# Kernel tuning notes

Hardware: AMD Instinct MI355X
Metric: run time of the kernel (lower is better)

## Reference

```python
import jax, jax.numpy as jnp
import numpy as np

HEADS = 16
IN_FEATURE = 1024
D_HEAD = IN_FEATURE // HEADS
N = 32768


def setup_inputs() -> dict:
    key = jax.random.key(0)
    ks = jax.random.split(key, 16)
    s_in = 1.0 / np.sqrt(IN_FEATURE)
    inp = {
        "Q": jax.random.normal(ks[0], (N, IN_FEATURE), jnp.float32),
        "K": jax.random.normal(ks[1], (N, IN_FEATURE), jnp.float32),
        "V": jax.random.normal(ks[2], (N, IN_FEATURE), jnp.float32),
        "lq_w": jax.random.uniform(ks[3], (D_HEAD, IN_FEATURE), jnp.float32, -s_in, s_in),
        "lq_b": jax.random.uniform(ks[4], (D_HEAD,), jnp.float32, -s_in, s_in),
        "lk1_w": jax.random.uniform(ks[5], (D_HEAD, IN_FEATURE), jnp.float32, -s_in, s_in),
        "lk1_b": jax.random.uniform(ks[6], (D_HEAD,), jnp.float32, -s_in, s_in),
        "lk2_w": jax.random.uniform(ks[7], (D_HEAD, IN_FEATURE), jnp.float32, -s_in, s_in),
        "lk2_b": jax.random.uniform(ks[8], (D_HEAD,), jnp.float32, -s_in, s_in),
        "lv1_w": jax.random.uniform(ks[9], (D_HEAD, IN_FEATURE), jnp.float32, -s_in, s_in),
        "lv1_b": jax.random.uniform(ks[10], (D_HEAD,), jnp.float32, -s_in, s_in),
        "lv2_w": jax.random.uniform(ks[11], (D_HEAD, IN_FEATURE), jnp.float32, -s_in, s_in),
        "lv2_b": jax.random.uniform(ks[12], (D_HEAD,), jnp.float32, -s_in, s_in),
        "lh_w": jax.random.uniform(ks[13], (IN_FEATURE, IN_FEATURE), jnp.float32, -s_in, s_in),
        "lh_b": jax.random.uniform(ks[14], (IN_FEATURE,), jnp.float32, -s_in, s_in),
    }
    return inp


def _linear(x, w, b):
    # torch nn.Linear: x @ w.T + b
    return x @ w.T + b


def reference(Q, K, V, lq_w, lq_b, lk1_w, lk1_b, lk2_w, lk2_b,
              lv1_w, lv1_b, lv2_w, lv2_b, lh_w, lh_b):
    # The original loops over heads but the body is loop-invariant:
    # every iteration produces the identical [N, D_HEAD] tensor.
    # Compute once and tile HEADS times (same math as the torch code).
    q = _linear(Q, lq_w, lq_b)     # [N, Dh]
    k1 = _linear(K, lk1_w, lk1_b)  # [N, Dh]
    k2 = _linear(V, lk2_w, lk2_b)
    v1 = _linear(K, lv1_w, lv1_b)
    v2 = _linear(V, lv2_w, lv2_b)

    kv1 = jnp.sum(q * k1, axis=1, keepdims=True)  # [N, 1]
    kv2 = jnp.sum(q * k2, axis=1, keepdims=True)  # [N, 1]
    m = jnp.maximum(kv1, kv2)
    e1 = jnp.exp(kv1 - m)
    e2 = jnp.exp(kv2 - m)
    denom = e1 + e2
    head = (e1 / denom) * v1 + (e2 / denom) * v2   # [N, Dh]

    concat_head = jnp.tile(head, (1, HEADS))       # [N, IN_FEATURE]
    return _linear(concat_head, lh_w, lh_b)
```

## Files before the change

kernel.cpp:

```cpp
#include <hip/hip_runtime.h>
#include <hip/hip_bf16.h>

typedef __attribute__((ext_vector_type(4))) float f32x4;
typedef __attribute__((ext_vector_type(8))) short bf16x8;

#define MFMA(a, b, c) __builtin_amdgcn_mfma_f32_16x16x32_bf16(a, b, c, 0, 0, 0)

__device__ __forceinline__ short f2bf(float f) {
    union { float f; unsigned u; } v; v.f = f;
    unsigned r = v.u + 0x7fffu + ((v.u >> 16) & 1u);
    return (short)(r >> 16);
}

__device__ __forceinline__ short f2bf_h(float f) {
    __hip_bfloat16 h = __float2bfloat16(f);
    return *reinterpret_cast<const short*>(&h);
}

__device__ __forceinline__ bf16x8 cvt8h(f32x4 a, f32x4 b) {
    bf16x8 r;
    #pragma unroll
    for (int i = 0; i < 4; ++i) {
        r[i]     = f2bf_h(a[i]);
        r[4 + i] = f2bf_h(b[i]);
    }
    return r;
}

__device__ __forceinline__ void gll16(const void* g, const void* l) {
    __builtin_amdgcn_global_load_lds(
        (const __attribute__((address_space(1))) void*)g,
        (__attribute__((address_space(3))) void*)l, 16, 0, 0);
}

#define WS_WEFF   327680
#define WS_BALL_B 786432

__global__ __launch_bounds__(256) void prep_kernel(
        const float* __restrict__ lq_w, const float* __restrict__ lk1_w,
        const float* __restrict__ lk2_w, const float* __restrict__ lv1_w,
        const float* __restrict__ lv2_w, const float* __restrict__ lh_w,
        const float* __restrict__ lq_b, const float* __restrict__ lk1_b,
        const float* __restrict__ lk2_b, const float* __restrict__ lv1_b,
        const float* __restrict__ lv2_b,
        short* __restrict__ W_all, short* __restrict__ weff,
        float* __restrict__ b_all) {
    int t = blockIdx.x * 256 + threadIdx.x;
    if (t < 327680) {
        int row = t >> 10, col = t & 1023;
        int seg = row >> 6, sr = row & 63;
        const float* src = (seg == 0) ? lq_w : (seg == 1) ? lk1_w
                         : (seg == 2) ? lv1_w : (seg == 3) ? lk2_w : lv2_w;
        W_all[t] = f2bf(src[sr * 1024 + col]);
    } else if (t < 393216) {
        int i = t - 327680;
        int j = i >> 6, d = i & 63;
        float s = 0.f;
        #pragma unroll
        for (int h = 0; h < 16; ++h) s += lh_w[j * 1024 + h * 64 + d];
        weff[i] = f2bf(s);
    } else if (t < 393536) {
        int i = t - 393216;
        int seg = i >> 6, si = i & 63;
        const float* src = (seg == 0) ? lq_b : (seg == 1) ? lk1_b
                         : (seg == 2) ? lv1_b : (seg == 3) ? lk2_b : lv2_b;
        b_all[i] = src[si];
    }
}

__global__ __launch_bounds__(256, 3) void fused_kernel(
        const float* __restrict__ Q, const float* __restrict__ K,
        const float* __restrict__ V, const short* __restrict__ W_all,
        const float* __restrict__ b_all, const short* __restrict__ weff,
        const float* __restrict__ lh_b, float* __restrict__ out) {
    __shared__ __align__(16) char lds[49152];
    const int tid  = threadIdx.x;
    const int wid  = tid >> 6;
    const int lane = tid & 63;
    const int lrow = lane & 15;
    const int lkg  = lane >> 4;
    const int RB   = blockIdx.x * 32;

    const float* asrc[3];
    int adst[3];
    #pragma unroll
    for (int u = 0; u < 3; ++u) {
        const int idx  = wid * 3 + u;
        const int inp  = idx >> 2;
        const int rg   = idx & 3;
        const int row  = rg * 8 + (lane >> 3);
        const int cell = lane & 7;
        const float* base = (inp == 0) ? Q : (inp == 1) ? K : V;
        asrc[u] = base + (size_t)(RB + row) * 1024 + ((cell ^ (row & 7)) << 2);
        adst[u] = inp * 4096 + rg * 1024;
    }

    const short* wsrc[5];
    #pragma unroll
    for (int j = 0; j < 5; ++j)
        wsrc[j] = W_all + (size_t)(j * 64 + wid * 16 + lrow) * 1024 + lkg * 8;

    f32x4 acc[2][5];
    #pragma unroll
    for (int rt = 0; rt < 2; ++rt)
        #pragma unroll
        for (int j = 0; j < 5; ++j) acc[rt][j] = (f32x4){0.f, 0.f, 0.f, 0.f};

    bf16x8 wE[5], wO[5];
    const int r7 = lrow & 7;
    const int c0 = ((lkg * 2)     ^ r7) << 4;
    const int c1 = ((lkg * 2 + 1) ^ r7) << 4;

    #pragma unroll
    for (int u = 0; u < 3; ++u) gll16(asrc[u], lds + adst[u]);
    #pragma unroll
    for (int j = 0; j < 5; ++j)
        asm volatile("global_load_dwordx4 %0, %1, off"
                     : "=&v"(wE[j]) : "v"(wsrc[j]) : "memory");
    #pragma unroll
    for (int j = 0; j < 5; ++j)
        asm volatile("global_load_dwordx4 %0, %1, off"
                     : "=&v"(wO[j]) : "v"(wsrc[j] + 32) : "memory");
    #pragma unroll
    for (int u = 0; u < 3; ++u) gll16(asrc[u] + 32, lds + 12288 + adst[u]);
    #pragma unroll
    for (int u = 0; u < 3; ++u) gll16(asrc[u] + 64, lds + 24576 + adst[u]);
    asm volatile("s_waitcnt vmcnt(11)" ::: "memory");
    __builtin_amdgcn_sched_barrier(0);
    __builtin_amdgcn_s_barrier();
    __builtin_amdgcn_sched_barrier(0);

#define BODY(c, wb)                                                            \
    {                                                                          \
        const char* Ab = lds + ((c) & 3) * 12288;                              \
        bf16x8 fq[2], fk[2], fv[2];                                            \
        _Pragma("unroll")                                                      \
        for (int rt = 0; rt < 2; ++rt) {                                       \
            const int ro = (rt * 16 + lrow) * 128;                             \
            f32x4 q0 = *(const f32x4*)(Ab + ro + c0);                          \
            f32x4 q1 = *(const f32x4*)(Ab + ro + c1);                          \
            f32x4 k0 = *(const f32x4*)(Ab + 4096 + ro + c0);                   \
            f32x4 k1 = *(const f32x4*)(Ab + 4096 + ro + c1);                   \
            f32x4 v0 = *(const f32x4*)(Ab + 8192 + ro + c0);                   \
            f32x4 v1 = *(const f32x4*)(Ab + 8192 + ro + c1);                   \
            fq[rt] = cvt8h(q0, q1);                                            \
            fk[rt] = cvt8h(k0, k1);                                            \
            fv[rt] = cvt8h(v0, v1);                                            \
        }                                                                      \
        _Pragma("unroll")                                                      \
        for (int rt = 0; rt < 2; ++rt) {                                       \
            acc[rt][0] = MFMA(fq[rt], wb[0], acc[rt][0]);                      \
            acc[rt][1] = MFMA(fk[rt], wb[1], acc[rt][1]);                      \
            acc[rt][2] = MFMA(fk[rt], wb[2], acc[rt][2]);                      \
            acc[rt][3] = MFMA(fv[rt], wb[3], acc[rt][3]);                      \
            acc[rt][4] = MFMA(fv[rt], wb[4], acc[rt][4]);                      \
        }                                                                      \
        const int kcW = ((c) + 2 < 32) ? ((c) + 2) : 31;                       \
        _Pragma("unroll")                                                      \
        for (int j = 0; j < 5; ++j)                                            \
            asm volatile("global_load_dwordx4 %0, %1, off"                     \
                         : "=&v"(wb[j]) : "v"(wsrc[j] + kcW * 32) : "memory"); \
        const int kcA = ((c) + 3 < 32) ? ((c) + 3) : 31;                       \
        char* Db = lds + (((c) + 3) & 3) * 12288;                              \
        _Pragma("unroll")                                                      \
        for (int u = 0; u < 3; ++u)                                            \
            gll16(asrc[u] + kcA * 32, Db + adst[u]);                           \
        __builtin_amdgcn_sched_barrier(0);                                     \
        asm volatile("s_waitcnt vmcnt(11)" ::: "memory");                      \
        __builtin_amdgcn_sched_barrier(0);                                     \
        __builtin_amdgcn_s_barrier();                                          \
        __builtin_amdgcn_sched_barrier(0);                                     \
    }

    #pragma unroll 1
    for (int cc = 0; cc < 32; cc += 2) {
        BODY(cc, wE);
        BODY(cc + 1, wO);
    }
#undef BODY

    asm volatile("s_waitcnt vmcnt(0)" ::: "memory");
    __builtin_amdgcn_sched_barrier(0);
    __syncthreads();

    float* epi = (float*)lds;
    #pragma unroll
    for (int rt = 0; rt < 2; ++rt)
        #pragma unroll
        for (int j = 0; j < 5; ++j) {
            const int col = j * 64 + wid * 16 + lrow;
            const float bb = b_all[col];
            #pragma unroll
            for (int i = 0; i < 4; ++i)
                epi[(rt * 16 + lkg * 4 + i) * 324 + col] = acc[rt][j][i] + bb;
        }
    __syncthreads();

    const int r = tid >> 3;
    const int p = tid & 7;
    const float* er = epi + r * 324;
    float p1 = 0.f, p2 = 0.f;
    #pragma unroll
    for (int jj = 0; jj < 8; ++jj) {
        const float qv = er[p * 8 + jj];
        p1 += qv * er[64  + p * 8 + jj];
        p2 += qv * er[192 + p * 8 + jj];
    }
    p1 += __shfl_xor(p1, 1, 64); p1 += __shfl_xor(p1, 2, 64); p1 += __shfl_xor(p1, 4, 64);
    p2 += __shfl_xor(p2, 1, 64); p2 += __shfl_xor(p2, 2, 64); p2 += __shfl_xor(p2, 4, 64);
    const float mx = fmaxf(p1, p2);
    const float e1 = __expf(p1 - mx);
    const float e2 = __expf(p2 - mx);
    const float inv = 1.f / (e1 + e2);
    const float g1 = e1 * inv, g2 = e2 * inv;

    short* head_s = (short*)(lds + 41472);
    #pragma unroll
    for (int d = 0; d < 8; ++d) {
        const float h = g1 * er[128 + p * 8 + d] + g2 * er[256 + p * 8 + d];
        head_s[r * 72 + p * 8 + d] = f2bf_h(h);
    }
    __syncthreads();

    bf16x8 ha[2][2];
    #pragma unroll
    for (int rt = 0; rt < 2; ++rt) {
        ha[rt][0] = *(const bf16x8*)(head_s + (rt * 16 + lrow) * 72 + lkg * 8);
        ha[rt][1] = *(const bf16x8*)(head_s + (rt * 16 + lrow) * 72 + 32 + lkg * 8);
    }
    const int cgbase = wid * 256;
    #pragma unroll 4
    for (int jt = 0; jt < 16; ++jt) {
        const int col = cgbase + jt * 16 + lrow;
        const float bb = lh_b[col];
        const short* wp = weff + col * 64 + lkg * 8;
        const bf16x8 w0 = *(const bf16x8*)(wp);
        const bf16x8 w1 = *(const bf16x8*)(wp + 32);
        #pragma unroll
        for (int rt = 0; rt < 2; ++rt) {
            f32x4 a = {bb, bb, bb, bb};
            a = MFMA(ha[rt][0], w0, a);
            a = MFMA(ha[rt][1], w1, a);
            #pragma unroll
            for (int i = 0; i < 4; ++i)
                out[(size_t)(RB + rt * 16 + lkg * 4 + i) * 1024 + col] = a[i];
        }
    }
}

extern "C" void kernel_launch(void* const* d_in, const int* in_sizes, int n_in,
                              void* d_out, int out_size, void* d_ws, size_t ws_size,
                              hipStream_t stream) {
    const float* Q     = (const float*)d_in[0];
    const float* K     = (const float*)d_in[1];
    const float* V     = (const float*)d_in[2];
    const float* lq_w  = (const float*)d_in[3];
    const float* lq_b  = (const float*)d_in[4];
    const float* lk1_w = (const float*)d_in[5];
    const float* lk1_b = (const float*)d_in[6];
    const float* lk2_w = (const float*)d_in[7];
    const float* lk2_b = (const float*)d_in[8];
    const float* lv1_w = (const float*)d_in[9];
    const float* lv1_b = (const float*)d_in[10];
    const float* lv2_w = (const float*)d_in[11];
    const float* lv2_b = (const float*)d_in[12];
    const float* lh_w  = (const float*)d_in[13];
    const float* lh_b  = (const float*)d_in[14];
    float* out = (float*)d_out;

    short* W_all = (short*)d_ws;
    short* weff  = W_all + WS_WEFF;
    float* b_all = (float*)((char*)d_ws + WS_BALL_B);

    prep_kernel<<<1538, 256, 0, stream>>>(lq_w, lk1_w, lk2_w, lv1_w, lv2_w, lh_w,
                                          lq_b, lk1_b, lk2_b, lv1_b, lv2_b,
                                          W_all, weff, b_all);
    fused_kernel<<<1024, 256, 0, stream>>>(Q, K, V, W_all, b_all, weff, lh_b, out);
}
```

Before: 163.7 us.

## Pre-swizzle projection weights into MFMA fragment order and reorder prefetch issue

The prep kernel now writes the five projection weight matrices in bf16 MFMA fragment order, so each lane's 16-byte weight fragment for a k-chunk sits contiguously and a wave reads one coalesced block per chunk instead of strided rows. The main loop now issues the activation LDS prefetch at the top of each step, before the LDS reads and MFMAs, with the weight register prefetch issued after. The vmcnt wait thresholds are changed to match the new issue order. This aims to cut weight-load transaction overhead and overlap activation loads better, at the risk of getting the counter bookkeeping wrong.

After: 140.0 us. -14.5%, faster.

```diff
diff --git a/kernel.cpp b/kernel.cpp
--- a/kernel.cpp
+++ b/kernel.cpp
@@ -43,21 +43,29 @@
         const float* __restrict__ lq_b, const float* __restrict__ lk1_b,
         const float* __restrict__ lk2_b, const float* __restrict__ lv1_b,
         const float* __restrict__ lv2_b,
-        short* __restrict__ W_all, short* __restrict__ weff,
+        short* __restrict__ W_frag, short* __restrict__ weff,
         float* __restrict__ b_all) {
     int t = blockIdx.x * 256 + threadIdx.x;
     if (t < 327680) {
-        int row = t >> 10, col = t & 1023;
-        int seg = row >> 6, sr = row & 63;
-        const float* src = (seg == 0) ? lq_w : (seg == 1) ? lk1_w
-                         : (seg == 2) ? lv1_w : (seg == 3) ? lk2_w : lv2_w;
-        W_all[t] = f2bf(src[sr * 1024 + col]);
+        const int e    = t & 7;
+        const int u16  = t >> 3;
+        const int lane = u16 & 63;
+        const int tl   = u16 >> 6;
+        const int c    = tl / 20;
+        const int tt   = tl - c * 20;
+        const int j    = tt >> 2;
+        const int wd   = tt & 3;
+        const int lrow = lane & 15;
+        const int lkg  = lane >> 4;
+        const float* src = (j == 0) ? lq_w : (j == 1) ? lk1_w
+                         : (j == 2) ? lv1_w : (j == 3) ? lk2_w : lv2_w;
+        W_frag[t] = f2bf(src[(wd * 16 + lrow) * 1024 + c * 32 + lkg * 8 + e]);
     } else if (t < 393216) {
         int i = t - 327680;
-        int j = i >> 6, d = i & 63;
+        int jj = i >> 6, d = i & 63;
         float s = 0.f;
         #pragma unroll
-        for (int h = 0; h < 16; ++h) s += lh_w[j * 1024 + h * 64 + d];
+        for (int h = 0; h < 16; ++h) s += lh_w[jj * 1024 + h * 64 + d];
         weff[i] = f2bf(s);
     } else if (t < 393536) {
         int i = t - 393216;
@@ -70,7 +78,7 @@
 
 __global__ __launch_bounds__(256, 3) void fused_kernel(
         const float* __restrict__ Q, const float* __restrict__ K,
-        const float* __restrict__ V, const short* __restrict__ W_all,
+        const float* __restrict__ V, const short* __restrict__ W_frag,
         const float* __restrict__ b_all, const short* __restrict__ weff,
         const float* __restrict__ lh_b, float* __restrict__ out) {
     __shared__ __align__(16) char lds[49152];
@@ -85,20 +93,20 @@
     int adst[3];
     #pragma unroll
     for (int u = 0; u < 3; ++u) {
-        const int idx  = wid * 3 + u;
-        const int inp  = idx >> 2;
-        const int rg   = idx & 3;
-        const int row  = rg * 8 + (lane >> 3);
-        const int cell = lane & 7;
+        const int i   = wid * 3 + u;
+        const int inp = i >> 2;
+        const int rg  = i & 3;
+        const int row = rg * 8 + (lane >> 3);
+        const int gc  = (lane & 7) ^ (row & 7);
         const float* base = (inp == 0) ? Q : (inp == 1) ? K : V;
-        asrc[u] = base + (size_t)(RB + row) * 1024 + ((cell ^ (row & 7)) << 2);
+        asrc[u] = base + (size_t)(RB + row) * 1024 + gc * 4;
         adst[u] = inp * 4096 + rg * 1024;
     }
 
     const short* wsrc[5];
     #pragma unroll
     for (int j = 0; j < 5; ++j)
-        wsrc[j] = W_all + (size_t)(j * 64 + wid * 16 + lrow) * 1024 + lkg * 8;
+        wsrc[j] = W_frag + (size_t)((j * 4 + wid) * 64 + lane) * 8;
 
     f32x4 acc[2][5];
     #pragma unroll
@@ -106,33 +114,41 @@
         #pragma unroll
         for (int j = 0; j < 5; ++j) acc[rt][j] = (f32x4){0.f, 0.f, 0.f, 0.f};
 
-    bf16x8 wE[5], wO[5];
+    bf16x8 wA[5], wB[5];
     const int r7 = lrow & 7;
     const int c0 = ((lkg * 2)     ^ r7) << 4;
     const int c1 = ((lkg * 2 + 1) ^ r7) << 4;
 
+#define GLD4(dst, p) \
+    asm volatile("global_load_dwordx4 %0, %1, off" : "=&v"(dst) : "v"(p) : "memory")
+
     #pragma unroll
     for (int u = 0; u < 3; ++u) gll16(asrc[u], lds + adst[u]);
     #pragma unroll
-    for (int j = 0; j < 5; ++j)
-        asm volatile("global_load_dwordx4 %0, %1, off"
-                     : "=&v"(wE[j]) : "v"(wsrc[j]) : "memory");
-    #pragma unroll
-    for (int j = 0; j < 5; ++j)
-        asm volatile("global_load_dwordx4 %0, %1, off"
-                     : "=&v"(wO[j]) : "v"(wsrc[j] + 32) : "memory");
-    #pragma unroll
     for (int u = 0; u < 3; ++u) gll16(asrc[u] + 32, lds + 12288 + adst[u]);
     #pragma unroll
+    for (int j = 0; j < 5; ++j) GLD4(wA[j], wsrc[j]);
+    #pragma unroll
     for (int u = 0; u < 3; ++u) gll16(asrc[u] + 64, lds + 24576 + adst[u]);
-    asm volatile("s_waitcnt vmcnt(11)" ::: "memory");
+    #pragma unroll
+    for (int j = 0; j < 5; ++j) GLD4(wB[j], wsrc[j] + 10240);
+    asm volatile("s_waitcnt vmcnt(8)" ::: "memory");
     __builtin_amdgcn_sched_barrier(0);
     __builtin_amdgcn_s_barrier();
     __builtin_amdgcn_sched_barrier(0);
 
-#define BODY(c, wb)                                                            \
+#define BODY(C, WB)                                                            \
     {                                                                          \
-        const char* Ab = lds + ((c) & 3) * 12288;                              \
+                                        \
+        const int kcA = ((C) + 3 <= 31) ? (C) + 3 : 31;                        \
+        char* Db = lds + (((C) + 3) & 3) * 12288;                              \
+        _Pragma("unroll")                                                      \
+        for (int u = 0; u < 3; ++u) gll16(asrc[u] + kcA * 32, Db + adst[u]);   \
+                                        \
+        asm volatile("s_waitcnt vmcnt(11)" ::: "memory");                      \
+        __builtin_amdgcn_sched_barrier(0);                                     \
+                                            \
+        const char* Ab = lds + ((C) & 3) * 12288;                              \
         bf16x8 fq[2], fk[2], fv[2];                                            \
         _Pragma("unroll")                                                      \
         for (int rt = 0; rt < 2; ++rt) {                                       \
@@ -149,24 +165,20 @@
         }                                                                      \
         _Pragma("unroll")                                                      \
         for (int rt = 0; rt < 2; ++rt) {                                       \
-            acc[rt][0] = MFMA(fq[rt], wb[0], acc[rt][0]);                      \
-            acc[rt][1] = MFMA(fk[rt], wb[1], acc[rt][1]);                      \
-            acc[rt][2] = MFMA(fk[rt], wb[2], acc[rt][2]);                      \
-            acc[rt][3] = MFMA(fv[rt], wb[3], acc[rt][3]);                      \
-            acc[rt][4] = MFMA(fv[rt], wb[4], acc[rt][4]);                      \
+            acc[rt][0] = MFMA(fq[rt], WB[0], acc[rt][0]);                      \
+            acc[rt][1] = MFMA(fk[rt], WB[1], acc[rt][1]);                      \
+            acc[rt][2] = MFMA(fk[rt], WB[2], acc[rt][2]);                      \
+            acc[rt][3] = MFMA(fv[rt], WB[3], acc[rt][3]);                      \
+            acc[rt][4] = MFMA(fv[rt], WB[4], acc[rt][4]);                      \
         }                                                                      \
-        const int kcW = ((c) + 2 < 32) ? ((c) + 2) : 31;                       \
+                                \
+        const int kcW = ((C) + 2 <= 31) ? (C) + 2 : 31;                        \
         _Pragma("unroll")                                                      \
         for (int j = 0; j < 5; ++j)                                            \
-            asm volatile("global_load_dwordx4 %0, %1, off"                     \
-                         : "=&v"(wb[j]) : "v"(wsrc[j] + kcW * 32) : "memory"); \
-        const int kcA = ((c) + 3 < 32) ? ((c) + 3) : 31;                       \
-        char* Db = lds + (((c) + 3) & 3) * 12288;                              \
-        _Pragma("unroll")                                                      \
-        for (int u = 0; u < 3; ++u)                                            \
-            gll16(asrc[u] + kcA * 32, Db + adst[u]);                           \
-        __builtin_amdgcn_sched_barrier(0);                                     \
-        asm volatile("s_waitcnt vmcnt(11)" ::: "memory");                      \
+            GLD4(WB[j], wsrc[j] + kcW * 10240);                                \
+                    \
+        __builtin_amdgcn_sched_barrier(0);                                     \
+        asm volatile("s_waitcnt vmcnt(8)" ::: "memory");                       \
         __builtin_amdgcn_sched_barrier(0);                                     \
         __builtin_amdgcn_s_barrier();                                          \
         __builtin_amdgcn_sched_barrier(0);                                     \
@@ -174,10 +186,11 @@
 
     #pragma unroll 1
     for (int cc = 0; cc < 32; cc += 2) {
-        BODY(cc, wE);
-        BODY(cc + 1, wO);
+        BODY(cc, wA)
+        BODY(cc + 1, wB)
     }
 #undef BODY
+#undef GLD4
 
     asm volatile("s_waitcnt vmcnt(0)" ::: "memory");
     __builtin_amdgcn_sched_barrier(0);
@@ -268,12 +281,12 @@
     const float* lh_b  = (const float*)d_in[14];
     float* out = (float*)d_out;
 
-    short* W_all = (short*)d_ws;
-    short* weff  = W_all + WS_WEFF;
-    float* b_all = (float*)((char*)d_ws + WS_BALL_B);
+    short* W_frag = (short*)d_ws;
+    short* weff   = W_frag + WS_WEFF;
+    float* b_all  = (float*)((char*)d_ws + WS_BALL_B);
 
     prep_kernel<<<1538, 256, 0, stream>>>(lq_w, lk1_w, lk2_w, lv1_w, lv2_w, lh_w,
                                           lq_b, lk1_b, lk2_b, lv1_b, lv2_b,
-                                          W_all, weff, b_all);
-    fused_kernel<<<1024, 256, 0, stream>>>(Q, K, V, W_all, b_all, weff, lh_b, out);
-}
+                                          W_frag, weff, b_all);
+    fused_kernel<<<1024, 256, 0, stream>>>(Q, K, V, W_frag, b_all, weff, lh_b, out);
+}
```
